# Kernel optimization log

Hardware: AMD Instinct MI355X
Metric: run time of the kernel (lower is better)

Reference implementation:

```python
import jax, jax.numpy as jnp
import numpy as np

DIMS, HEAD, FREQ = 1024, 16, 10000
HEAD_DIM = DIMS // HEAD          # 64
ROT = HEAD_DIM // 2              # 32
B, S = 4, 8192


def setup_inputs() -> dict:
    key = jax.random.key(0)
    k1, k2, k3, k4 = jax.random.split(key, 4)
    x = jax.random.normal(k1, (B, S, DIMS), dtype=jnp.float32)
    matrix = jax.random.normal(k2, (HEAD_DIM, HEAD_DIM), dtype=jnp.float32)
    thetas = jax.random.normal(k3, (ROT,), dtype=jnp.float32) * 0.1
    tscale = jnp.ones((1,), dtype=jnp.float32)
    # inverse frequencies exactly as in __init__
    invf = (1.0 / FREQ ** (jnp.arange(0, HEAD_DIM, 2, dtype=jnp.float32) / HEAD_DIM)).astype(jnp.float32)
    pairs = jax.random.randint(k4, (ROT, 2), 0, HEAD_DIM, dtype=jnp.int32)
    return {"x": x, "matrix": matrix, "thetas": thetas, "tscale": tscale,
            "invf": invf, "pairs": pairs}


def _composed_rotation(thetas, tscale, pairs, d, dtype):
    # Build every Givens matrix G_k (same element-set order as the torch code)
    theta = thetas * tscale[0]

    def make_G(i, j, th):
        c, sn = jnp.cos(th), jnp.sin(th)
        G = jnp.eye(d, dtype=dtype)
        return G.at[i, i].set(c).at[j, j].set(c).at[i, j].set(-sn).at[j, i].set(sn)

    Gs = jax.vmap(make_G)(pairs[:, 0], pairs[:, 1], theta)  # [rot, d, d]

    def step(acc, G):
        return acc @ G, None

    G_comb, _ = jax.lax.scan(step, jnp.eye(d, dtype=dtype), Gs)
    return G_comb


def reference(x, matrix, thetas, tscale, invf, pairs):
    b, s, dims = x.shape
    d = matrix.shape[0]          # head_dim
    h = dims // d                # heads

    G_comb = _composed_rotation(thetas, tscale, pairs, d, x.dtype)

    xr = x.reshape(b, s, h, d)
    # flat @ G_combined @ self.matrix (acts on last dim)
    xr = xr @ (G_comb @ matrix)

    # sinusoidal RoPE: sinusoid[s, d/2] = pos * invf
    pos = jnp.arange(s, dtype=x.dtype)
    sinusoid = pos[:, None] * invf[None, :]
    sin = jnp.sin(sinusoid)[None, :, None, :]   # [1, s, 1, d/2]
    cos = jnp.cos(sinusoid)[None, :, None, :]

    x1, x2 = xr[..., ::2], xr[..., 1::2]
    out = jnp.concatenate([x1 * cos - x2 * sin, x1 * sin + x2 * cos], axis=-1)
    return out.reshape(b, s, dims) * jnp.asarray(np.sqrt(dims), x.dtype)
```

## Files before the change

kernel.cpp:

```cpp
#include <hip/hip_runtime.h>
#include <math.h>

#define BB 4
#define SS 8192
#define HH 16
#define DD 64
#define ROT 32
#define NG (BB * SS * HH)
#define RPB 128
#define LSTR 65

__global__ void setup_G(const float* __restrict__ thetas,
                        const float* __restrict__ tscale,
                        const int* __restrict__ pairs,
                        float* __restrict__ G) {
  __shared__ float Gs[DD][DD];
  const int t = threadIdx.x;
  for (int c = 0; c < DD; ++c) Gs[t][c] = (t == c) ? 1.0f : 0.0f;
  const float ts = tscale[0];
  for (int r = 0; r < ROT; ++r) {
    const int i = pairs[2 * r], j = pairs[2 * r + 1];
    const float th = thetas[r] * ts;
    const float cc = cosf(th), sn = sinf(th);
    if (i == j) {
      Gs[t][i] *= sn;
    } else {
      const float a = Gs[t][i], b = Gs[t][j];
      Gs[t][i] = a * cc + b * sn;
      Gs[t][j] = b * cc - a * sn;
    }
  }
  for (int c = 0; c < DD; ++c) G[t * DD + c] = Gs[t][c];
}

__global__ void setup_Mk(const float* __restrict__ G,
                         const float* __restrict__ matrix,
                         float* __restrict__ M) {
  const int e = blockIdx.x * 256 + threadIdx.x;
  const int row = e >> 6, col = e & 63;
  float a0 = 0.f, a1 = 0.f, a2 = 0.f, a3 = 0.f;
  for (int k = 0; k < DD; k += 4) {
    a0 = fmaf(G[row * DD + k], matrix[k * DD + col], a0);
    a1 = fmaf(G[row * DD + k + 1], matrix[(k + 1) * DD + col], a1);
    a2 = fmaf(G[row * DD + k + 2], matrix[(k + 2) * DD + col], a2);
    a3 = fmaf(G[row * DD + k + 3], matrix[(k + 3) * DD + col], a3);
  }
  M[e] = (a0 + a1) + (a2 + a3);
}

__global__ void setup_table(const float* __restrict__ invf,
                            float* __restrict__ tab) {
  const int idx = blockIdx.x * 256 + threadIdx.x;
  if (idx >= SS * 32) return;
  const int s = idx >> 5, d = idx & 31;
  const float ang = (float)s * invf[d];
  tab[s * 64 + d] = 32.0f * cosf(ang);
  tab[s * 64 + 32 + d] = 32.0f * sinf(ang);
}

__global__ __launch_bounds__(256) void apply_rot(
    const float* __restrict__ x, const float* __restrict__ M,
    const float* __restrict__ tab, const float* __restrict__ invf,
    float* __restrict__ out) {
  __shared__ float lds[RPB * LSTR];
  const int tid = threadIdx.x;
  const size_t R0 = (size_t)blockIdx.x * RPB;

  const float4* __restrict__ xg = (const float4*)x + R0 * 16;
#pragma unroll
  for (int i = 0; i < 8; ++i) {
    const int f = i * 256 + tid;
    const int row = f >> 4, c4 = f & 15;
    const float4 v = xg[f];
    *(float4*)&lds[row * LSTR + c4 * 4] = v;
  }
  __syncthreads();

  const int r = tid & (RPB - 1);
  const int h = __builtin_amdgcn_readfirstlane(tid >> 7);
  const float* __restrict__ Mh = M + h * 32;
  const float* __restrict__ xr = &lds[r * LSTR];

  float acc[32];
#pragma unroll
  for (int c = 0; c < 32; ++c) acc[c] = 0.0f;

  for (int k4 = 0; k4 < 16; ++k4) {
    const float4 xv = *(const float4*)&xr[k4 * 4];
    const float* __restrict__ m0 = Mh + k4 * 4 * DD;
#pragma unroll
    for (int c = 0; c < 32; ++c) acc[c] = fmaf(xv.x, m0[c], acc[c]);
#pragma unroll
    for (int c = 0; c < 32; ++c) acc[c] = fmaf(xv.y, m0[DD + c], acc[c]);
#pragma unroll
    for (int c = 0; c < 32; ++c) acc[c] = fmaf(xv.z, m0[2 * DD + c], acc[c]);
#pragma unroll
    for (int c = 0; c < 32; ++c) acc[c] = fmaf(xv.w, m0[3 * DD + c], acc[c]);
  }

  const int g = (int)R0 + r;
  const int spos = (g >> 4) & (SS - 1);
  float cz[16], sz[16];
  if (tab) {
    const float4* __restrict__ tc = (const float4*)(tab + spos * 64 + h * 16);
    const float4* __restrict__ tn =
        (const float4*)(tab + spos * 64 + 32 + h * 16);
#pragma unroll
    for (int q = 0; q < 4; ++q) {
      *(float4*)&cz[4 * q] = tc[q];
      *(float4*)&sz[4 * q] = tn[q];
    }
  } else {
#pragma unroll
    for (int d = 0; d < 16; ++d) {
      const float ang = (float)spos * invf[h * 16 + d];
      cz[d] = 32.0f * cosf(ang);
      sz[d] = 32.0f * sinf(ang);
    }
  }

  float lo[16], hi[16];
#pragma unroll
  for (int d = 0; d < 16; ++d) {
    const float e = acc[2 * d], o = acc[2 * d + 1];
    lo[d] = e * cz[d] - o * sz[d];
    hi[d] = e * sz[d] + o * cz[d];
  }

  __syncthreads();
  float* __restrict__ orow = &lds[r * LSTR];
#pragma unroll
  for (int q = 0; q < 4; ++q) {
    *(float4*)&orow[16 * h + 4 * q] = *(float4*)&lo[4 * q];
    *(float4*)&orow[32 + 16 * h + 4 * q] = *(float4*)&hi[4 * q];
  }
  __syncthreads();

  float4* __restrict__ og = (float4*)out + R0 * 16;
#pragma unroll
  for (int i = 0; i < 8; ++i) {
    const int f = i * 256 + tid;
    const int row = f >> 4, c4 = f & 15;
    og[f] = *(float4*)&lds[row * LSTR + c4 * 4];
  }
}

extern "C" void kernel_launch(void* const* d_in, const int* in_sizes, int n_in,
                              void* d_out, int out_size, void* d_ws,
                              size_t ws_size, hipStream_t stream) {
  const float* x = (const float*)d_in[0];
  const float* matrix = (const float*)d_in[1];
  const float* thetas = (const float*)d_in[2];
  const float* tscale = (const float*)d_in[3];
  const float* invf = (const float*)d_in[4];
  const int* pairs = (const int*)d_in[5];
  float* out = (float*)d_out;

  float* G = (float*)d_ws;
  float* M = G + DD * DD;
  float* tab = M + DD * DD;
  const size_t need = (size_t)(2 * DD * DD + SS * 64) * sizeof(float);
  const bool have_tab = ws_size >= need;

  setup_G<<<1, 64, 0, stream>>>(thetas, tscale, pairs, G);
  setup_Mk<<<16, 256, 0, stream>>>(G, matrix, M);
  if (have_tab) setup_table<<<(SS * 32) / 256, 256, 0, stream>>>(invf, tab);
  apply_rot<<<NG / RPB, 256, 0, stream>>>(x, M, have_tab ? tab : nullptr, invf,
                                          out);
}
```

Before: 285.2 us.

## Split per-row output columns across 512 threads and fuse setup kernels

The main kernel now uses 512 threads per block with four head-quarters per row. Each thread accumulates 16 output columns instead of 32, which halves the per-thread accumulator and cos/sin registers and adds more waves to hide latency. The G-construction and G·matrix setup kernels are merged into one launch that keeps G in shared memory, removing a launch and a global round-trip. The cost is that each of the 16 setup blocks redundantly recomputes G, and the stricter launch bounds may cap registers.

After: 281.5 us. About the same (-1.3%).

```diff
diff --git a/kernel.cpp b/kernel.cpp
--- a/kernel.cpp
+++ b/kernel.cpp
@@ -9,41 +9,40 @@
 #define NG (BB * SS * HH)
 #define RPB 128
 #define LSTR 65
+#define TPB 512
 
-__global__ void setup_G(const float* __restrict__ thetas,
-                        const float* __restrict__ tscale,
-                        const int* __restrict__ pairs,
-                        float* __restrict__ G) {
+__global__ void setup_GM(const float* __restrict__ thetas,
+                         const float* __restrict__ tscale,
+                         const int* __restrict__ pairs,
+                         const float* __restrict__ matrix,
+                         float* __restrict__ M) {
   __shared__ float Gs[DD][DD];
   const int t = threadIdx.x;
-  for (int c = 0; c < DD; ++c) Gs[t][c] = (t == c) ? 1.0f : 0.0f;
-  const float ts = tscale[0];
-  for (int r = 0; r < ROT; ++r) {
-    const int i = pairs[2 * r], j = pairs[2 * r + 1];
-    const float th = thetas[r] * ts;
-    const float cc = cosf(th), sn = sinf(th);
-    if (i == j) {
-      Gs[t][i] *= sn;
-    } else {
-      const float a = Gs[t][i], b = Gs[t][j];
-      Gs[t][i] = a * cc + b * sn;
-      Gs[t][j] = b * cc - a * sn;
+  if (t < DD) {
+    for (int c = 0; c < DD; ++c) Gs[t][c] = (t == c) ? 1.0f : 0.0f;
+    const float ts = tscale[0];
+    for (int r = 0; r < ROT; ++r) {
+      const int i = pairs[2 * r], j = pairs[2 * r + 1];
+      const float th = thetas[r] * ts;
+      const float cc = cosf(th), sn = sinf(th);
+      if (i == j) {
+        Gs[t][i] *= sn;
+      } else {
+        const float a = Gs[t][i], b = Gs[t][j];
+        Gs[t][i] = a * cc + b * sn;
+        Gs[t][j] = b * cc - a * sn;
+      }
     }
   }
-  for (int c = 0; c < DD; ++c) G[t * DD + c] = Gs[t][c];
-}
-
-__global__ void setup_Mk(const float* __restrict__ G,
-                         const float* __restrict__ matrix,
-                         float* __restrict__ M) {
-  const int e = blockIdx.x * 256 + threadIdx.x;
+  __syncthreads();
+  const int e = blockIdx.x * 256 + t;
   const int row = e >> 6, col = e & 63;
   float a0 = 0.f, a1 = 0.f, a2 = 0.f, a3 = 0.f;
   for (int k = 0; k < DD; k += 4) {
-    a0 = fmaf(G[row * DD + k], matrix[k * DD + col], a0);
-    a1 = fmaf(G[row * DD + k + 1], matrix[(k + 1) * DD + col], a1);
-    a2 = fmaf(G[row * DD + k + 2], matrix[(k + 2) * DD + col], a2);
-    a3 = fmaf(G[row * DD + k + 3], matrix[(k + 3) * DD + col], a3);
+    a0 = fmaf(Gs[row][k], matrix[k * DD + col], a0);
+    a1 = fmaf(Gs[row][k + 1], matrix[(k + 1) * DD + col], a1);
+    a2 = fmaf(Gs[row][k + 2], matrix[(k + 2) * DD + col], a2);
+    a3 = fmaf(Gs[row][k + 3], matrix[(k + 3) * DD + col], a3);
   }
   M[e] = (a0 + a1) + (a2 + a3);
 }
@@ -58,7 +57,7 @@
   tab[s * 64 + 32 + d] = 32.0f * sinf(ang);
 }
 
-__global__ __launch_bounds__(256) void apply_rot(
+__global__ __launch_bounds__(TPB, 8) void apply_rot(
     const float* __restrict__ x, const float* __restrict__ M,
     const float* __restrict__ tab, const float* __restrict__ invf,
     float* __restrict__ out) {
@@ -68,8 +67,8 @@
 
   const float4* __restrict__ xg = (const float4*)x + R0 * 16;
 #pragma unroll
-  for (int i = 0; i < 8; ++i) {
-    const int f = i * 256 + tid;
+  for (int i = 0; i < 4; ++i) {
+    const int f = i * TPB + tid;
     const int row = f >> 4, c4 = f & 15;
     const float4 v = xg[f];
     *(float4*)&lds[row * LSTR + c4 * 4] = v;
@@ -78,70 +77,70 @@
 
   const int r = tid & (RPB - 1);
   const int h = __builtin_amdgcn_readfirstlane(tid >> 7);
-  const float* __restrict__ Mh = M + h * 32;
+  const float* __restrict__ Mh = M + h * 16;
   const float* __restrict__ xr = &lds[r * LSTR];
 
-  float acc[32];
+  float acc[16];
 #pragma unroll
-  for (int c = 0; c < 32; ++c) acc[c] = 0.0f;
+  for (int c = 0; c < 16; ++c) acc[c] = 0.0f;
 
+#pragma unroll 4
   for (int k4 = 0; k4 < 16; ++k4) {
     const float4 xv = *(const float4*)&xr[k4 * 4];
     const float* __restrict__ m0 = Mh + k4 * 4 * DD;
 #pragma unroll
-    for (int c = 0; c < 32; ++c) acc[c] = fmaf(xv.x, m0[c], acc[c]);
+    for (int c = 0; c < 16; ++c) acc[c] = fmaf(xv.x, m0[c], acc[c]);
 #pragma unroll
-    for (int c = 0; c < 32; ++c) acc[c] = fmaf(xv.y, m0[DD + c], acc[c]);
+    for (int c = 0; c < 16; ++c) acc[c] = fmaf(xv.y, m0[DD + c], acc[c]);
 #pragma unroll
-    for (int c = 0; c < 32; ++c) acc[c] = fmaf(xv.z, m0[2 * DD + c], acc[c]);
+    for (int c = 0; c < 16; ++c) acc[c] = fmaf(xv.z, m0[2 * DD + c], acc[c]);
 #pragma unroll
-    for (int c = 0; c < 32; ++c) acc[c] = fmaf(xv.w, m0[3 * DD + c], acc[c]);
+    for (int c = 0; c < 16; ++c) acc[c] = fmaf(xv.w, m0[3 * DD + c], acc[c]);
   }
 
   const int g = (int)R0 + r;
   const int spos = (g >> 4) & (SS - 1);
-  float cz[16], sz[16];
+  float cz[8], sz[8];
   if (tab) {
-    const float4* __restrict__ tc = (const float4*)(tab + spos * 64 + h * 16);
+    const float4* __restrict__ tc = (const float4*)(tab + spos * 64 + h * 8);
     const float4* __restrict__ tn =
-        (const float4*)(tab + spos * 64 + 32 + h * 16);
+        (const float4*)(tab + spos * 64 + 32 + h * 8);
 #pragma unroll
-    for (int q = 0; q < 4; ++q) {
+    for (int q = 0; q < 2; ++q) {
       *(float4*)&cz[4 * q] = tc[q];
       *(float4*)&sz[4 * q] = tn[q];
     }
   } else {
 #pragma unroll
-    for (int d = 0; d < 16; ++d) {
-      const float ang = (float)spos * invf[h * 16 + d];
+    for (int d = 0; d < 8; ++d) {
+      const float ang = (float)spos * invf[h * 8 + d];
       cz[d] = 32.0f * cosf(ang);
       sz[d] = 32.0f * sinf(ang);
     }
   }
 
-  float lo[16], hi[16];
-#pragma unroll
-  for (int d = 0; d < 16; ++d) {
-    const float e = acc[2 * d], o = acc[2 * d + 1];
-    lo[d] = e * cz[d] - o * sz[d];
-    hi[d] = e * sz[d] + o * cz[d];
-  }
-
   __syncthreads();
   float* __restrict__ orow = &lds[r * LSTR];
 #pragma unroll
-  for (int q = 0; q < 4; ++q) {
-    *(float4*)&orow[16 * h + 4 * q] = *(float4*)&lo[4 * q];
-    *(float4*)&orow[32 + 16 * h + 4 * q] = *(float4*)&hi[4 * q];
+  for (int q = 0; q < 2; ++q) {
+    float4 lo, hi;
+#pragma unroll
+    for (int d = 0; d < 4; ++d) {
+      const int dd = 4 * q + d;
+      const float e = acc[2 * dd], o = acc[2 * dd + 1];
+      ((float*)&lo)[d] = e * cz[dd] - o * sz[dd];
+      ((float*)&hi)[d] = e * sz[dd] + o * cz[dd];
+    }
+    *(float4*)&orow[8 * h + 4 * q] = lo;
+    *(float4*)&orow[32 + 8 * h + 4 * q] = hi;
   }
   __syncthreads();
 
   float4* __restrict__ og = (float4*)out + R0 * 16;
 #pragma unroll
-  for (int i = 0; i < 8; ++i) {
-    const int f = i * 256 + tid;
-    const int row = f >> 4, c4 = f & 15;
-    og[f] = *(float4*)&lds[row * LSTR + c4 * 4];
+  for (int i = 0; i < 4; ++i) {
+    const int f = i * TPB + tid;
+    og[f] = *(float4*)&lds[(f >> 4) * LSTR + (f & 15) * 4];
   }
 }
 
@@ -156,15 +155,13 @@
   const int* pairs = (const int*)d_in[5];
   float* out = (float*)d_out;
 
-  float* G = (float*)d_ws;
-  float* M = G + DD * DD;
+  float* M = (float*)d_ws;
   float* tab = M + DD * DD;
-  const size_t need = (size_t)(2 * DD * DD + SS * 64) * sizeof(float);
+  const size_t need = (size_t)(DD * DD + SS * 64) * sizeof(float);
   const bool have_tab = ws_size >= need;
 
-  setup_G<<<1, 64, 0, stream>>>(thetas, tscale, pairs, G);
-  setup_Mk<<<16, 256, 0, stream>>>(G, matrix, M);
+  setup_GM<<<16, 256, 0, stream>>>(thetas, tscale, pairs, matrix, M);
   if (have_tab) setup_table<<<(SS * 32) / 256, 256, 0, stream>>>(invf, tab);
-  apply_rot<<<NG / RPB, 256, 0, stream>>>(x, M, have_tab ? tab : nullptr, invf,
+  apply_rot<<<NG / RPB, TPB, 0, stream>>>(x, M, have_tab ? tab : nullptr, invf,
                                           out);
 }
```
